# Optimization experiments

Hardware: AMD Instinct MI355X
Metric: run time of the kernel (lower is better)

The kernel has to match this reference:

```python
import jax, jax.numpy as jnp
import numpy as np

CM = 0.05   # collision_margin
NT = 4      # n_timesteps

def _lin(x, W, b):
    return x @ W + b

def _mlp2(x, W1, b1, W2, b2):
    return _lin(jax.nn.relu(_lin(x, W1, b1)), W2, b2)

def _mlp3(x, W1, b1, W2, b2, W3, b3):
    h = jax.nn.relu(_lin(x, W1, b1))
    h = jax.nn.relu(_lin(h, W2, b2))
    return _lin(h, W3, b3)

def _xavier(key, fan_in, fan_out):
    std = np.sqrt(2.0 / (fan_in + fan_out))
    return jax.random.normal(key, (fan_in, fan_out), dtype=jnp.float32) * std

def setup_inputs() -> dict:
    key = jax.random.key(0)
    ks = jax.random.split(key, 16)
    sd, h, es, ud, rd, gd = 8, 128, 128, 32, 64, 32
    B, N, T = 16, 64, 8
    inp = {
        'states': jax.random.normal(ks[0], (B, N, T, sd), dtype=jnp.float32),
        'temp': 1,
        # StateEncoder: Linear(sd,h)-ReLU-Linear(h,es)-ReLU
        'sW1': _xavier(ks[1], sd, h), 'sb1': jnp.zeros((h,), jnp.float32),
        'sW2': _xavier(ks[2], h, es), 'sb2': jnp.zeros((es,), jnp.float32),
        # InputEncoder (collision_margin path): Linear(sd,h)-ReLU-Linear(h,ud)
        'uW1': _xavier(ks[3], sd, h), 'ub1': jnp.zeros((h,), jnp.float32),
        'uW2': _xavier(ks[4], h, ud), 'ub2': jnp.zeros((ud,), jnp.float32),
        # InputPropagator: Linear(es+ud, ud)
        'upW': _xavier(ks[5], es + ud, ud), 'upb': jnp.zeros((ud,), jnp.float32),
        # RelationEncoder (collision_margin path): Linear(sd,h)-ReLU-Linear(h,rd)
        'reW1': _xavier(ks[6], sd, h), 'reb1': jnp.zeros((h,), jnp.float32),
        'reW2': _xavier(ks[7], h, rd), 'reb2': jnp.zeros((rd,), jnp.float32),
        # RelationPropagator: Linear(2*es+rd, rd)
        'rpW': _xavier(ks[8], 2 * es + rd, rd), 'rpb': jnp.zeros((rd,), jnp.float32),
        # ComposedEmbedding: Linear(es+ud+rd,h)-ReLU-Linear(h,h)-ReLU-Linear(h,gd)
        'cW1': _xavier(ks[9], es + ud + rd, h), 'cb1': jnp.zeros((h,), jnp.float32),
        'cW2': _xavier(ks[10], h, h), 'cb2': jnp.zeros((h,), jnp.float32),
        'cW3': _xavier(ks[11], h, gd), 'cb3': jnp.zeros((gd,), jnp.float32),
    }
    return inp

def reference(states, temp, sW1, sb1, sW2, sb2, uW1, ub1, uW2, ub2, upW, upb,
              reW1, reb1, reW2, reb2, rpW, rpb, cW1, cb1, cW2, cb2, cW3, cb3):
    B, N, T, sd = states.shape
    BT = B * T
    s = states.transpose(0, 2, 1, 3).reshape(BT, N, sd)  # [BT,N,sd]

    # node encoders
    enc_obj = jax.nn.relu(_mlp2(s, sW1, sb1, sW2, sb2))   # [BT,N,es]
    enc_u = _mlp2(s, uW1, ub1, uW2, ub2)                  # [BT,N,ud] (no relu in collision_margin path)
    # u mask (get_u_states_mask)
    u = ((jnp.abs(s[..., 0:1]) > 1 - CM) | (jnp.abs(s[..., NT:NT + 1]) > 1 - CM)).astype(s.dtype)

    obs_u = jax.nn.relu(_lin(jnp.concatenate([enc_obj, enc_u], axis=-1), upW, upb))  # [BT,N,ud]
    enc_comp = jnp.concatenate([enc_obj, obs_u], axis=-1)  # [BT,N,es+ud]

    # pairwise relations: receiver i (dim1), sender j (dim2)
    rel_states = s[:, :, None, :] - s[:, None, :, :]        # [BT,N,N,sd]
    enc_rel = jax.nn.relu(_mlp2(rel_states, reW1, reb1, reW2, reb2))  # [BT,N,N,rd]
    sel = ((jnp.abs(rel_states[..., 0:1]) > 2 * CM) |
           (jnp.abs(rel_states[..., NT:NT + 1]) > 2 * CM)).astype(s.dtype)  # [BT,N,N,1]

    es = enc_obj.shape[-1]
    recv = jnp.broadcast_to(enc_obj[:, :, None, :], (BT, N, N, es))
    send = jnp.broadcast_to(enc_obj[:, None, :, :], (BT, N, N, es))
    rel_in = jnp.concatenate([recv, send, enc_rel], axis=-1)            # [BT,N,N,2es+rd]
    rel_eff = jax.nn.relu(_lin(rel_in, rpW, rpb)) * sel                 # [BT,N,N,rd]
    rel_agg = rel_eff.sum(axis=2)                                       # scatter-sum over senders -> [BT,N,rd]

    enc_comp = jnp.concatenate([enc_comp, rel_agg], axis=-1)            # [BT,N,es+ud+rd]
    g = _mlp3(enc_comp, cW1, cb1, cW2, cb2, cW3, cb3)                   # [BT,N,gd]
    return g.reshape(B, T, N, -1)
```

## Files before the change

kernel.cpp:

```cpp
#include <hip/hip_runtime.h>
#include <hip/hip_bf16.h>


typedef __bf16 bf16x8 __attribute__((ext_vector_type(8)));
typedef _Float16 half8 __attribute__((ext_vector_type(8)));
typedef _Float16 half4 __attribute__((ext_vector_type(4)));
typedef float f32x4 __attribute__((ext_vector_type(4)));

static __device__ __forceinline__ half8 relu8(half8 x) {
    half8 z = {};
    return __builtin_elementwise_max(x, z);
}

__global__ __launch_bounds__(256) void k_prep(
    const float* __restrict__ sW1, const float* __restrict__ uW1,
    const float* __restrict__ reW1, const float* __restrict__ sW2,
    const float* __restrict__ uW2, const float* __restrict__ upW,
    const float* __restrict__ reW2, const float* __restrict__ rpW,
    const float* __restrict__ cW1, const float* __restrict__ cW2,
    const float* __restrict__ cW3,
    __bf16* __restrict__ Wl1f, __bf16* __restrict__ Ws2f,
    __bf16* __restrict__ Wu2f, __bf16* __restrict__ Wupf,
    __bf16* __restrict__ Wabf, _Float16* __restrict__ W2f,
    _Float16* __restrict__ Wbf, __bf16* __restrict__ Wc1f,
    __bf16* __restrict__ Wc2f, __bf16* __restrict__ Wc3f)
{
    const int tid  = blockIdx.x * 256 + threadIdx.x;
    const int nthr = gridDim.x * 256;

#define PACK(dst, CAST, NKT, NCT, EXPR)                             \
    for (int q = tid; q < (NKT) * (NCT) * 512; q += nthr) {         \
        const int f = q >> 9, rem = q & 511;                        \
        const int lane = rem >> 3, e = rem & 7;                     \
        const int kt = f / (NCT), ct = f % (NCT);                   \
        const int k = kt * 32 + (lane >> 4) * 8 + e;                \
        const int c = ct * 16 + (lane & 15);                        \
        (dst)[q] = (CAST)(EXPR);                                    \
        (void)k; (void)c;                                           \
    }

    PACK(Wl1f, __bf16, 1, 24, (k >= 8 ? 0.f :
        (c < 128 ? sW1[k * 128 + c] :
         c < 256 ? uW1[k * 128 + (c - 128)] : reW1[k * 128 + (c - 256)])))
    PACK(Ws2f, __bf16, 4, 8, sW2[k * 128 + c])
    PACK(Wu2f, __bf16, 4, 2, uW2[k * 32 + c])
    PACK(Wupf, __bf16, 5, 2, (k < 160 ? upW[k * 32 + c] : 0.f))
    PACK(Wabf, __bf16, 4, 8, (c < 64 ? rpW[k * 64 + c] : rpW[(128 + k) * 64 + (c - 64)]))
    PACK(W2f,  _Float16, 4, 4, reW2[k * 64 + c])
    PACK(Wbf,  _Float16, 2, 4, rpW[(256 + k) * 64 + c])
    PACK(Wc1f, __bf16, 7, 8, cW1[k * 128 + c])
    PACK(Wc2f, __bf16, 4, 8, cW2[k * 128 + c])
    PACK(Wc3f, __bf16, 4, 2, cW3[k * 32 + c])
#undef PACK
}

__global__ __launch_bounds__(512, 2) void k_mega(
    const float* __restrict__ states,
    const float* __restrict__ sb1, const float* __restrict__ sb2,
    const float* __restrict__ ub1, const float* __restrict__ ub2,
    const float* __restrict__ upb, const float* __restrict__ reb1,
    const float* __restrict__ reb2, const float* __restrict__ rpb,
    const float* __restrict__ cb1, const float* __restrict__ cb2,
    const float* __restrict__ cb3,
    const __bf16* __restrict__ Wl1f, const __bf16* __restrict__ Ws2f,
    const __bf16* __restrict__ Wu2f, const __bf16* __restrict__ Wupf,
    const __bf16* __restrict__ Wabf,
    const _Float16* __restrict__ W2f, const _Float16* __restrict__ Wbf,
    const __bf16* __restrict__ Wc1f, const __bf16* __restrict__ Wc2f,
    const __bf16* __restrict__ Wc3f,
    float* __restrict__ out)
{
    const int t    = threadIdx.x;
    const int lane = t & 63;
    const int w    = t >> 6;
    const int lr   = lane >> 4;
    const int lc   = lane & 15;
    const int bid  = (blockIdx.x & 7) * 64 + (blockIdx.x >> 3);
    const int bt   = bid >> 2;
    const int ig   = bid & 3;
    const int b    = bt >> 3, tstep = bt & 7;
    const int rowb = bt * 64 + ig * 16;

    __shared__ _Float16 s_pj[64 * 128];
    __shared__ _Float16 s_bmT[64 * 72];
    __shared__ float    s_ai[16 * 64];
    __shared__ __bf16   s_eo[64 * 128];
    __shared__ __bf16   s_scr[16 * 256];
    __shared__ __bf16   s_x[16 * 256];
    __shared__ __bf16   s_eu[16 * 40];
    __shared__ _Float16 s_rb[128];
    __shared__ float    s_s0[64], s_s4[64];

    if (t < 128) s_rb[t] = (_Float16)reb1[t];
    if (t < 64) {
        const float* sp = &states[((size_t)((b * 64 + t) * 8 + tstep)) * 8];
        s_s0[t] = sp[0];
        s_s4[t] = sp[4];
    }

    for (int rt = 0; rt < 4; ++rt) {
        bf16x8 af1 = {};
        if (lr == 0) {
            const int n = rt * 16 + lc;
            const float* sp = &states[((size_t)((b * 64 + n) * 8 + tstep)) * 8];
            const float4 v0 = *reinterpret_cast<const float4*>(sp);
            const float4 v1 = *reinterpret_cast<const float4*>(sp + 4);
            af1[0] = (__bf16)v0.x; af1[1] = (__bf16)v0.y;
            af1[2] = (__bf16)v0.z; af1[3] = (__bf16)v0.w;
            af1[4] = (__bf16)v1.x; af1[5] = (__bf16)v1.y;
            af1[6] = (__bf16)v1.z; af1[7] = (__bf16)v1.w;
        }
        const int nct = (rt == ig) ? 3 : 2;
        for (int ci = 0; ci < nct; ++ci) {
            const int ct = (ci < 2) ? (w * 2 + ci) : (16 + w);
            const int wl = (ct < 8) ? ct : (ct < 16 ? ct + 8 : ct - 8);
            const bf16x8 wf = *reinterpret_cast<const bf16x8*>(
                Wl1f + ((size_t)(wl * 64 + lane)) * 8);
            const float bias = (ct < 8) ? sb1[ct * 16 + lc]
                              : (ct >= 16) ? ub1[(ct - 16) * 16 + lc] : 0.f;
            f32x4 acc = {bias, bias, bias, bias};
            acc = __builtin_amdgcn_mfma_f32_16x16x32_bf16(af1, wf, acc, 0, 0, 0);
            #pragma unroll
            for (int r = 0; r < 4; ++r) {
                const int jj = lr * 4 + r;
                if (ct < 8) {
                    const int col = ct * 16 + lc, g = col >> 3;
                    s_scr[jj * 256 + (((g ^ (jj & 7)) << 3) | (col & 7))] =
                        (__bf16)fmaxf(acc[r], 0.f);
                } else if (ct < 16) {
                    const int col = (ct - 8) * 16 + lc, g = col >> 3;
                    const int j64 = rt * 16 + jj;
                    s_pj[j64 * 128 + ((g ^ (j64 & 7)) << 3) + (col & 7)] =
                        (_Float16)acc[r];
                } else {
                    const int col = 128 + (ct - 16) * 16 + lc, g = col >> 3;
                    s_scr[jj * 256 + (((g ^ (jj & 7)) << 3) | (col & 7))] =
                        (__bf16)fmaxf(acc[r], 0.f);
                }
            }
        }
        __syncthreads();

        {
            const int jr = lc, sw = lc & 7;
            bf16x8 h1f[4];
            #pragma unroll
            for (int kt = 0; kt < 4; ++kt)
                h1f[kt] = *reinterpret_cast<const bf16x8*>(
                    &s_scr[jr * 256 + (((kt * 4 + lr) ^ sw) << 3)]);
            const int ct = w;
            const float bias = sb2[ct * 16 + lc];
            f32x4 acc = {bias, bias, bias, bias};
            #pragma unroll
            for (int kt = 0; kt < 4; ++kt) {
                const bf16x8 wf = *reinterpret_cast<const bf16x8*>(
                    Ws2f + ((size_t)((kt * 8 + ct) * 64 + lane)) * 8);
                acc = __builtin_amdgcn_mfma_f32_16x16x32_bf16(h1f[kt], wf, acc, 0, 0, 0);
            }
            #pragma unroll
            for (int r = 0; r < 4; ++r) {
                const int jj = lr * 4 + r;
                const int j64 = rt * 16 + jj;
                const int col = ct * 16 + lc, g = col >> 3;
                const __bf16 v = (__bf16)fmaxf(acc[r], 0.f);
                s_eo[j64 * 128 + (((g ^ (j64 & 7)) << 3) | (col & 7))] = v;
                if (rt == ig)
                    s_x[jj * 256 + (((g ^ (jj & 7)) << 3) | (col & 7))] = v;
            }
            if (rt == ig && w < 2) {
                bf16x8 huf[4];
                #pragma unroll
                for (int kt = 0; kt < 4; ++kt)
                    huf[kt] = *reinterpret_cast<const bf16x8*>(
                        &s_scr[jr * 256 + (((16 + kt * 4 + lr) ^ sw) << 3)]);
                const float bias2 = ub2[w * 16 + lc];
                f32x4 acc2 = {bias2, bias2, bias2, bias2};
                #pragma unroll
                for (int kt = 0; kt < 4; ++kt) {
                    const bf16x8 wf = *reinterpret_cast<const bf16x8*>(
                        Wu2f + ((size_t)((kt * 2 + w) * 64 + lane)) * 8);
                    acc2 = __builtin_amdgcn_mfma_f32_16x16x32_bf16(huf[kt], wf, acc2, 0, 0, 0);
                }
                #pragma unroll
                for (int r = 0; r < 4; ++r)
                    s_eu[(lr * 4 + r) * 40 + w * 16 + lc] = (__bf16)acc2[r];
            }
        }
        __syncthreads();
    }

    {
        #pragma unroll
        for (int q = 0; q < 2; ++q) {
            const int task = w * 2 + q;
            const int rt2 = task >> 2;
            const int ct = 4 + (task & 3);
            const int j64 = rt2 * 16 + lc, so = j64 & 7;
            bf16x8 eof[4];
            #pragma unroll
            for (int kt = 0; kt < 4; ++kt)
                eof[kt] = *reinterpret_cast<const bf16x8*>(
                    &s_eo[j64 * 128 + (((kt * 4 + lr) ^ so) << 3)]);
            f32x4 acc = {0.f, 0.f, 0.f, 0.f};
            #pragma unroll
            for (int kt = 0; kt < 4; ++kt) {
                const bf16x8 wf = *reinterpret_cast<const bf16x8*>(
                    Wabf + ((size_t)((kt * 8 + ct) * 64 + lane)) * 8);
                acc = __builtin_amdgcn_mfma_f32_16x16x32_bf16(eof[kt], wf, acc, 0, 0, 0);
            }
            #pragma unroll
            for (int r = 0; r < 4; ++r)
                s_bmT[((ct - 4) * 16 + lc) * 72 + rt2 * 16 + lr * 4 + r] =
                    (_Float16)acc[r];
        }
        const int jo = ig * 16 + lc, so2 = jo & 7;
        if (w < 4) {
            bf16x8 eof[4];
            #pragma unroll
            for (int kt = 0; kt < 4; ++kt)
                eof[kt] = *reinterpret_cast<const bf16x8*>(
                    &s_eo[jo * 128 + (((kt * 4 + lr) ^ so2) << 3)]);
            f32x4 acc = {0.f, 0.f, 0.f, 0.f};
            #pragma unroll
            for (int kt = 0; kt < 4; ++kt) {
                const bf16x8 wf = *reinterpret_cast<const bf16x8*>(
                    Wabf + ((size_t)((kt * 8 + w) * 64 + lane)) * 8);
                acc = __builtin_amdgcn_mfma_f32_16x16x32_bf16(eof[kt], wf, acc, 0, 0, 0);
            }
            #pragma unroll
            for (int r = 0; r < 4; ++r) {
                const int col = w * 16 + lc;
                s_ai[(lr * 4 + r) * 64 + col] = acc[r] + rpb[col];
            }
        } else if (w < 6) {
            const int ct = w - 4;
            bf16x8 eof[5];
            #pragma unroll
            for (int kt = 0; kt < 4; ++kt)
                eof[kt] = *reinterpret_cast<const bf16x8*>(
                    &s_eo[jo * 128 + (((kt * 4 + lr) ^ so2) << 3)]);
            eof[4] = *reinterpret_cast<const bf16x8*>(&s_eu[lc * 40 + lr * 8]);
            const float bias = upb[ct * 16 + lc];
            f32x4 acc = {bias, bias, bias, bias};
            #pragma unroll
            for (int kt = 0; kt < 5; ++kt) {
                const bf16x8 wf = *reinterpret_cast<const bf16x8*>(
                    Wupf + ((size_t)((kt * 2 + ct) * 64 + lane)) * 8);
                acc = __builtin_amdgcn_mfma_f32_16x16x32_bf16(eof[kt], wf, acc, 0, 0, 0);
            }
            #pragma unroll
            for (int r = 0; r < 4; ++r) {
                const int jj = lr * 4 + r;
                const int col = 128 + ct * 16 + lc, g = col >> 3;
                s_x[jj * 256 + (((g ^ (jj & 7)) << 3) | (col & 7))] =
                    (__bf16)fmaxf(acc[r], 0.f);
            }
        }
    }
    __syncthreads();

    half8 w2f[4][4];
    #pragma unroll
    for (int kt = 0; kt < 4; ++kt)
        #pragma unroll
        for (int ct = 0; ct < 4; ++ct)
            w2f[kt][ct] = *reinterpret_cast<const half8*>(
                W2f + ((size_t)((kt * 4 + ct) * 64 + lane)) * 8);
    half8 wbf[2][4];
    #pragma unroll
    for (int kt = 0; kt < 2; ++kt)
        #pragma unroll
        for (int ct = 0; ct < 4; ++ct)
            wbf[kt][ct] = *reinterpret_cast<const half8*>(
                Wbf + ((size_t)((kt * 4 + ct) * 64 + lane)) * 8);
    float reb2c[4];
    #pragma unroll
    for (int ct = 0; ct < 4; ++ct) reb2c[ct] = reb2[ct * 16 + lc];

    _Float16* er = reinterpret_cast<_Float16*>(s_eo) + w * (16 * 64);
    float rag2[2][4];

    for (int q = 0; q < 2; ++q) {
        const int il = w * 2 + q;
        const int i  = ig * 16 + il;
        const int isw = i & 7;

        half8 pib[4];
        #pragma unroll
        for (int kt = 0; kt < 4; ++kt) {
            const int g = kt * 4 + lr;
            const half8 pv = *reinterpret_cast<const half8*>(
                &s_pj[i * 128 + ((g ^ isw) << 3)]);
            const half8 rb = *reinterpret_cast<const half8*>(&s_rb[g * 8]);
            pib[kt] = pv + rb;
        }
        float aic[4];
        #pragma unroll
        for (int ct = 0; ct < 4; ++ct) aic[ct] = s_ai[il * 64 + ct * 16 + lc];
        const unsigned long long selm = __ballot(
            fabsf(s_s0[i] - s_s0[lane]) > 0.1f ||
            fabsf(s_s4[i] - s_s4[lane]) > 0.1f);

        float ragg[4] = {0.f, 0.f, 0.f, 0.f};

        for (int jt = 0; jt < 4; ++jt) {
            const int j = jt * 16 + lc;
            const int jsw = j & 7;
            half8 af[4];
            #pragma unroll
            for (int kt = 0; kt < 4; ++kt) {
                const int g = (kt * 4 + lr) ^ jsw;
                const half8 pj = *reinterpret_cast<const half8*>(
                    &s_pj[j * 128 + (g << 3)]);
                af[kt] = relu8(pib[kt] - pj);
            }
            #pragma unroll
            for (int ct = 0; ct < 4; ++ct) {
                f32x4 acc = {reb2c[ct], reb2c[ct], reb2c[ct], reb2c[ct]};
                #pragma unroll
                for (int kt = 0; kt < 4; ++kt)
                    acc = __builtin_amdgcn_mfma_f32_16x16x32_f16(
                        af[kt], w2f[kt][ct], acc, 0, 0, 0);
                #pragma unroll
                for (int r = 0; r < 4; ++r) {
                    const int jj2 = lr * 4 + r;
                    const int c = ct * 16 + lc;
                    er[jj2 * 64 + ((((c >> 3) ^ (jj2 & 7)) << 3) | (c & 7))] =
                        (_Float16)fmaxf(acc[r], 0.f);
                }
            }
            half8 a2[2];
            #pragma unroll
            for (int kt = 0; kt < 2; ++kt) {
                const int g = (kt * 4 + lr) ^ (lc & 7);
                a2[kt] = *reinterpret_cast<const half8*>(&er[lc * 64 + (g << 3)]);
            }
            #pragma unroll
            for (int ct = 0; ct < 4; ++ct) {
                const half4 bm4 = *reinterpret_cast<const half4*>(
                    &s_bmT[(ct * 16 + lc) * 72 + jt * 16 + lr * 4]);
                f32x4 acc = {aic[ct] + (float)bm4[0], aic[ct] + (float)bm4[1],
                             aic[ct] + (float)bm4[2], aic[ct] + (float)bm4[3]};
                #pragma unroll
                for (int kt = 0; kt < 2; ++kt)
                    acc = __builtin_amdgcn_mfma_f32_16x16x32_f16(
                        a2[kt], wbf[kt][ct], acc, 0, 0, 0);
                #pragma unroll
                for (int r = 0; r < 4; ++r) {
                    const int jj = jt * 16 + lr * 4 + r;
                    float v = fmaxf(acc[r], 0.f);
                    v = ((selm >> jj) & 1ull) ? v : 0.f;
                    ragg[ct] += v;
                }
            }
        }
        #pragma unroll
        for (int ct = 0; ct < 4; ++ct) {
            ragg[ct] += __shfl_xor(ragg[ct], 16);
            ragg[ct] += __shfl_xor(ragg[ct], 32);
            rag2[q][ct] = ragg[ct];
        }
    }
    if (lr == 0) {
        #pragma unroll
        for (int q = 0; q < 2; ++q) {
            const int il = w * 2 + q;
            #pragma unroll
            for (int ct = 0; ct < 4; ++ct) {
                const int c = ct * 16 + lc;
                const int gg = 20 + (c >> 3);
                s_x[il * 256 + ((gg ^ (il & 7)) << 3) + (c & 7)] =
                    (__bf16)rag2[q][ct];
            }
        }
    }
    __syncthreads();

    __bf16* s_h1 = s_scr;
    __bf16* s_h2 = s_scr + 16 * 128;

    const int jr = lc;
    const int sw = lc & 7;
    bf16x8 xf[7];
    #pragma unroll
    for (int kt = 0; kt < 7; ++kt)
        xf[kt] = *reinterpret_cast<const bf16x8*>(
            &s_x[jr * 256 + (((kt * 4 + lr) ^ sw) << 3)]);
    {
        const int ct = w;
        const float bias = cb1[ct * 16 + lc];
        f32x4 acc = {bias, bias, bias, bias};
        #pragma unroll
        for (int kt = 0; kt < 7; ++kt) {
            const bf16x8 wf = *reinterpret_cast<const bf16x8*>(
                Wc1f + ((size_t)((kt * 8 + ct) * 64 + lane)) * 8);
            acc = __builtin_amdgcn_mfma_f32_16x16x32_bf16(xf[kt], wf, acc, 0, 0, 0);
        }
        #pragma unroll
        for (int r = 0; r < 4; ++r) {
            const int jj = lr * 4 + r;
            const int col = ct * 16 + lc, g = col >> 3;
            s_h1[jj * 128 + (((g ^ (jj & 7)) << 3) | (col & 7))] =
                (__bf16)fmaxf(acc[r], 0.f);
        }
    }
    __syncthreads();

    {
        bf16x8 hf[4];
        #pragma unroll
        for (int kt = 0; kt < 4; ++kt)
            hf[kt] = *reinterpret_cast<const bf16x8*>(
                &s_h1[jr * 128 + (((kt * 4 + lr) ^ sw) << 3)]);
        const int ct = w;
        const float bias = cb2[ct * 16 + lc];
        f32x4 acc = {bias, bias, bias, bias};
        #pragma unroll
        for (int kt = 0; kt < 4; ++kt) {
            const bf16x8 wf = *reinterpret_cast<const bf16x8*>(
                Wc2f + ((size_t)((kt * 8 + ct) * 64 + lane)) * 8);
            acc = __builtin_amdgcn_mfma_f32_16x16x32_bf16(hf[kt], wf, acc, 0, 0, 0);
        }
        #pragma unroll
        for (int r = 0; r < 4; ++r) {
            const int jj = lr * 4 + r;
            const int col = ct * 16 + lc, g = col >> 3;
            s_h2[jj * 128 + (((g ^ (jj & 7)) << 3) | (col & 7))] =
                (__bf16)fmaxf(acc[r], 0.f);
        }
    }
    __syncthreads();

    if (w < 2) {
        bf16x8 h2f[4];
        #pragma unroll
        for (int kt = 0; kt < 4; ++kt)
            h2f[kt] = *reinterpret_cast<const bf16x8*>(
                &s_h2[jr * 128 + (((kt * 4 + lr) ^ sw) << 3)]);
        const int ct = w;
        const float bias = cb3[ct * 16 + lc];
        f32x4 acc = {bias, bias, bias, bias};
        #pragma unroll
        for (int kt = 0; kt < 4; ++kt) {
            const bf16x8 wf = *reinterpret_cast<const bf16x8*>(
                Wc3f + ((size_t)((kt * 2 + ct) * 64 + lane)) * 8);
            acc = __builtin_amdgcn_mfma_f32_16x16x32_bf16(h2f[kt], wf, acc, 0, 0, 0);
        }
        #pragma unroll
        for (int r = 0; r < 4; ++r) {
            const int rg = rowb + lr * 4 + r;
            out[(size_t)rg * 32 + ct * 16 + lc] = acc[r];
        }
    }
}

extern "C" void kernel_launch(void* const* d_in, const int* in_sizes, int n_in,
                              void* d_out, int out_size, void* d_ws, size_t ws_size,
                              hipStream_t stream) {
    const float* states = (const float*)d_in[0];
    const float* sW1  = (const float*)d_in[2];
    const float* sb1  = (const float*)d_in[3];
    const float* sW2  = (const float*)d_in[4];
    const float* sb2  = (const float*)d_in[5];
    const float* uW1  = (const float*)d_in[6];
    const float* ub1  = (const float*)d_in[7];
    const float* uW2  = (const float*)d_in[8];
    const float* ub2  = (const float*)d_in[9];
    const float* upW  = (const float*)d_in[10];
    const float* upb  = (const float*)d_in[11];
    const float* reW1 = (const float*)d_in[12];
    const float* reb1 = (const float*)d_in[13];
    const float* reW2 = (const float*)d_in[14];
    const float* reb2 = (const float*)d_in[15];
    const float* rpW  = (const float*)d_in[16];
    const float* rpb  = (const float*)d_in[17];
    const float* cW1  = (const float*)d_in[18];
    const float* cb1  = (const float*)d_in[19];
    const float* cW2  = (const float*)d_in[20];
    const float* cb2  = (const float*)d_in[21];
    const float* cW3  = (const float*)d_in[22];
    const float* cb3  = (const float*)d_in[23];
    float* out = (float*)d_out;

    _Float16* W2f  = (_Float16*)d_ws;
    _Float16* Wbf  = W2f + 16 * 512;
    __bf16* Wl1f = (__bf16*)(Wbf + 8 * 512);
    __bf16* Ws2f = Wl1f + 24 * 512;
    __bf16* Wu2f = Ws2f + 32 * 512;
    __bf16* Wupf = Wu2f + 8 * 512;
    __bf16* Wabf = Wupf + 10 * 512;
    __bf16* Wc1f = Wabf + 32 * 512;
    __bf16* Wc2f = Wc1f + 56 * 512;
    __bf16* Wc3f = Wc2f + 32 * 512;

    k_prep<<<64, 256, 0, stream>>>(sW1, uW1, reW1, sW2, uW2, upW, reW2, rpW,
                                   cW1, cW2, cW3,
                                   Wl1f, Ws2f, Wu2f, Wupf, Wabf, W2f, Wbf,
                                   Wc1f, Wc2f, Wc3f);
    k_mega<<<512, 512, 0, stream>>>(states, sb1, sb2, ub1, ub2, upb,
                                    reb1, reb2, rpb, cb1, cb2, cb3,
                                    Wl1f, Ws2f, Wu2f, Wupf, Wabf, W2f, Wbf,
                                    Wc1f, Wc2f, Wc3f, out);
}
```

Baseline: 152.2 us.

## Double-buffer node-encoder scratch, pad LDS rows, stage Wb weights in LDS

Replaces the separate shared arrays with one manually laid-out LDS block and double-buffers the encoder scratch. The next row tile's first layer now runs alongside the current tile's second layer, halving the barriers in the node-encoder loop. Swizzled LDS indexing for s_pj and the per-wave relation scratch is replaced by padded row strides. The rpW tail fragments are read from LDS instead of being held in registers, which cuts register pressure. s_setprio is also raised around the pairwise MFMA loop, at the cost of more LDS traffic and possible bank conflicts from the padded layout.

Result: faster. 146.2 us (-3.9%).

```diff
diff --git a/kernel.cpp b/kernel.cpp
--- a/kernel.cpp
+++ b/kernel.cpp
@@ -53,6 +53,19 @@
     PACK(Wc3f, __bf16, 4, 2, cW3[k * 32 + c])
 #undef PACK
 }
+
+constexpr int OFF_PJ   = 0;
+constexpr int OFF_BMT  = 17408;
+constexpr int OFF_AI   = 26624;
+constexpr int OFF_EO   = 30720;
+constexpr int OFF_SCRA = 47104;
+constexpr int OFF_SCRB = 55296;
+constexpr int OFF_X    = 63488;
+constexpr int OFF_EU   = 71680;
+constexpr int OFF_RB   = 72960;
+constexpr int OFF_S0   = 73216;
+constexpr int OFF_S4   = 73472;
+constexpr int LDS_SZ   = 73728;
 
 __global__ __launch_bounds__(512, 2) void k_mega(
     const float* __restrict__ states,
@@ -70,6 +83,8 @@
     const __bf16* __restrict__ Wc3f,
     float* __restrict__ out)
 {
+    __shared__ __align__(16) char lds[LDS_SZ];
+
     const int t    = threadIdx.x;
     const int lane = t & 63;
     const int w    = t >> 6;
@@ -81,24 +96,26 @@
     const int b    = bt >> 3, tstep = bt & 7;
     const int rowb = bt * 64 + ig * 16;
 
-    __shared__ _Float16 s_pj[64 * 128];
-    __shared__ _Float16 s_bmT[64 * 72];
-    __shared__ float    s_ai[16 * 64];
-    __shared__ __bf16   s_eo[64 * 128];
-    __shared__ __bf16   s_scr[16 * 256];
-    __shared__ __bf16   s_x[16 * 256];
-    __shared__ __bf16   s_eu[16 * 40];
-    __shared__ _Float16 s_rb[128];
-    __shared__ float    s_s0[64], s_s4[64];
-
-    if (t < 128) s_rb[t] = (_Float16)reb1[t];
+    _Float16* s_pjh = (_Float16*)(lds + OFF_PJ);
+    _Float16* s_bmT = (_Float16*)(lds + OFF_BMT);
+    float*    s_ai  = (float*)(lds + OFF_AI);
+    __bf16*   s_eo  = (__bf16*)(lds + OFF_EO);
+    __bf16*   scrA  = (__bf16*)(lds + OFF_SCRA);
+    __bf16*   scrB  = (__bf16*)(lds + OFF_SCRB);
+    __bf16*   s_x   = (__bf16*)(lds + OFF_X);
+    __bf16*   s_eu  = (__bf16*)(lds + OFF_EU);
+    _Float16* s_rbh = (_Float16*)(lds + OFF_RB);
+    float*    s_s0  = (float*)(lds + OFF_S0);
+    float*    s_s4  = (float*)(lds + OFF_S4);
+
+    if (t < 128) s_rbh[t] = (_Float16)reb1[t];
     if (t < 64) {
         const float* sp = &states[((size_t)((b * 64 + t) * 8 + tstep)) * 8];
         s_s0[t] = sp[0];
         s_s4[t] = sp[4];
     }
 
-    for (int rt = 0; rt < 4; ++rt) {
+    auto do_N1 = [&](int rt, __bf16* scr) {
         bf16x8 af1 = {};
         if (lr == 0) {
             const int n = rt * 16 + lc;
@@ -125,67 +142,72 @@
                 const int jj = lr * 4 + r;
                 if (ct < 8) {
                     const int col = ct * 16 + lc, g = col >> 3;
-                    s_scr[jj * 256 + (((g ^ (jj & 7)) << 3) | (col & 7))] =
+                    scr[jj * 256 + (((g ^ (jj & 7)) << 3) | (col & 7))] =
                         (__bf16)fmaxf(acc[r], 0.f);
                 } else if (ct < 16) {
-                    const int col = (ct - 8) * 16 + lc, g = col >> 3;
-                    const int j64 = rt * 16 + jj;
-                    s_pj[j64 * 128 + ((g ^ (j64 & 7)) << 3) + (col & 7)] =
+                    s_pjh[(rt * 16 + jj) * 136 + (ct - 8) * 16 + lc] =
                         (_Float16)acc[r];
                 } else {
                     const int col = 128 + (ct - 16) * 16 + lc, g = col >> 3;
-                    s_scr[jj * 256 + (((g ^ (jj & 7)) << 3) | (col & 7))] =
+                    scr[jj * 256 + (((g ^ (jj & 7)) << 3) | (col & 7))] =
                         (__bf16)fmaxf(acc[r], 0.f);
                 }
             }
         }
-        __syncthreads();
-
-        {
-            const int jr = lc, sw = lc & 7;
-            bf16x8 h1f[4];
+    };
+    auto do_N2 = [&](int rt, __bf16* scr) {
+        const int jr = lc, sw = lc & 7;
+        bf16x8 h1f[4];
+        #pragma unroll
+        for (int kt = 0; kt < 4; ++kt)
+            h1f[kt] = *reinterpret_cast<const bf16x8*>(
+                &scr[jr * 256 + (((kt * 4 + lr) ^ sw) << 3)]);
+        const int ct = w;
+        const float bias = sb2[ct * 16 + lc];
+        f32x4 acc = {bias, bias, bias, bias};
+        #pragma unroll
+        for (int kt = 0; kt < 4; ++kt) {
+            const bf16x8 wf = *reinterpret_cast<const bf16x8*>(
+                Ws2f + ((size_t)((kt * 8 + ct) * 64 + lane)) * 8);
+            acc = __builtin_amdgcn_mfma_f32_16x16x32_bf16(h1f[kt], wf, acc, 0, 0, 0);
+        }
+        #pragma unroll
+        for (int r = 0; r < 4; ++r) {
+            const int jj = lr * 4 + r;
+            const int j64 = rt * 16 + jj;
+            const int col = ct * 16 + lc, g = col >> 3;
+            const __bf16 v = (__bf16)fmaxf(acc[r], 0.f);
+            s_eo[j64 * 128 + (((g ^ (j64 & 7)) << 3) | (col & 7))] = v;
+            if (rt == ig)
+                s_x[jj * 256 + (((g ^ (jj & 7)) << 3) | (col & 7))] = v;
+        }
+        if (rt == ig && w < 2) {
+            bf16x8 huf[4];
             #pragma unroll
             for (int kt = 0; kt < 4; ++kt)
-                h1f[kt] = *reinterpret_cast<const bf16x8*>(
-                    &s_scr[jr * 256 + (((kt * 4 + lr) ^ sw) << 3)]);
-            const int ct = w;
-            const float bias = sb2[ct * 16 + lc];
-            f32x4 acc = {bias, bias, bias, bias};
+                huf[kt] = *reinterpret_cast<const bf16x8*>(
+                    &scr[jr * 256 + (((16 + kt * 4 + lr) ^ sw) << 3)]);
+            const float bias2 = ub2[w * 16 + lc];
+            f32x4 acc2 = {bias2, bias2, bias2, bias2};
             #pragma unroll
             for (int kt = 0; kt < 4; ++kt) {
                 const bf16x8 wf = *reinterpret_cast<const bf16x8*>(
-                    Ws2f + ((size_t)((kt * 8 + ct) * 64 + lane)) * 8);
-                acc = __builtin_amdgcn_mfma_f32_16x16x32_bf16(h1f[kt], wf, acc, 0, 0, 0);
-            }
-            #pragma unroll
-            for (int r = 0; r < 4; ++r) {
-                const int jj = lr * 4 + r;
-                const int j64 = rt * 16 + jj;
-                const int col = ct * 16 + lc, g = col >> 3;
-                const __bf16 v = (__bf16)fmaxf(acc[r], 0.f);
-                s_eo[j64 * 128 + (((g ^ (j64 & 7)) << 3) | (col & 7))] = v;
-                if (rt == ig)
-                    s_x[jj * 256 + (((g ^ (jj & 7)) << 3) | (col & 7))] = v;
-            }
-            if (rt == ig && w < 2) {
-                bf16x8 huf[4];
-                #pragma unroll
-                for (int kt = 0; kt < 4; ++kt)
-                    huf[kt] = *reinterpret_cast<const bf16x8*>(
-                        &s_scr[jr * 256 + (((16 + kt * 4 + lr) ^ sw) << 3)]);
-                const float bias2 = ub2[w * 16 + lc];
-                f32x4 acc2 = {bias2, bias2, bias2, bias2};
-                #pragma unroll
-                for (int kt = 0; kt < 4; ++kt) {
-                    const bf16x8 wf = *reinterpret_cast<const bf16x8*>(
-                        Wu2f + ((size_t)((kt * 2 + w) * 64 + lane)) * 8);
-                    acc2 = __builtin_amdgcn_mfma_f32_16x16x32_bf16(huf[kt], wf, acc2, 0, 0, 0);
-                }
-                #pragma unroll
-                for (int r = 0; r < 4; ++r)
-                    s_eu[(lr * 4 + r) * 40 + w * 16 + lc] = (__bf16)acc2[r];
-            }
-        }
+                    Wu2f + ((size_t)((kt * 2 + w) * 64 + lane)) * 8);
+                acc2 = __builtin_amdgcn_mfma_f32_16x16x32_bf16(huf[kt], wf, acc2, 0, 0, 0);
+            }
+            #pragma unroll
+            for (int r = 0; r < 4; ++r)
+                s_eu[(lr * 4 + r) * 40 + w * 16 + lc] = (__bf16)acc2[r];
+        }
+    };
+
+    do_N1(0, scrA);
+    __syncthreads();
+    for (int rt = 0; rt < 4; ++rt) {
+        __bf16* cur = (rt & 1) ? scrB : scrA;
+        __bf16* nxt = (rt & 1) ? scrA : scrB;
+        do_N2(rt, cur);
+        if (rt < 3) do_N1(rt + 1, nxt);
         __syncthreads();
     }
 
@@ -256,6 +278,8 @@
                     (__bf16)fmaxf(acc[r], 0.f);
             }
         }
+        *reinterpret_cast<half8*>((_Float16*)scrB + t * 8) =
+            *reinterpret_cast<const half8*>(Wbf + t * 8);
     }
     __syncthreads();
 
@@ -266,34 +290,26 @@
         for (int ct = 0; ct < 4; ++ct)
             w2f[kt][ct] = *reinterpret_cast<const half8*>(
                 W2f + ((size_t)((kt * 4 + ct) * 64 + lane)) * 8);
-    half8 wbf[2][4];
-    #pragma unroll
-    for (int kt = 0; kt < 2; ++kt)
-        #pragma unroll
-        for (int ct = 0; ct < 4; ++ct)
-            wbf[kt][ct] = *reinterpret_cast<const half8*>(
-                Wbf + ((size_t)((kt * 4 + ct) * 64 + lane)) * 8);
     float reb2c[4];
     #pragma unroll
     for (int ct = 0; ct < 4; ++ct) reb2c[ct] = reb2[ct * 16 + lc];
 
-    _Float16* er = reinterpret_cast<_Float16*>(s_eo) + w * (16 * 64);
+    const _Float16* wbl = (const _Float16*)scrB;
+    _Float16* er = (_Float16*)s_eo + w * (16 * 88);
+    const int erw = (lr * 4) * 88 + lc;
+    const int erd = lc * 88 + lr * 8;
     float rag2[2][4];
 
     for (int q = 0; q < 2; ++q) {
         const int il = w * 2 + q;
         const int i  = ig * 16 + il;
-        const int isw = i & 7;
-
+
+        const _Float16* pirow = s_pjh + i * 136;
         half8 pib[4];
         #pragma unroll
-        for (int kt = 0; kt < 4; ++kt) {
-            const int g = kt * 4 + lr;
-            const half8 pv = *reinterpret_cast<const half8*>(
-                &s_pj[i * 128 + ((g ^ isw) << 3)]);
-            const half8 rb = *reinterpret_cast<const half8*>(&s_rb[g * 8]);
-            pib[kt] = pv + rb;
-        }
+        for (int kt = 0; kt < 4; ++kt)
+            pib[kt] = *reinterpret_cast<const half8*>(pirow + kt * 32 + lr * 8)
+                    + *reinterpret_cast<const half8*>(s_rbh + kt * 32 + lr * 8);
         float aic[4];
         #pragma unroll
         for (int ct = 0; ct < 4; ++ct) aic[ct] = s_ai[il * 64 + ct * 16 + lc];
@@ -304,16 +320,13 @@
         float ragg[4] = {0.f, 0.f, 0.f, 0.f};
 
         for (int jt = 0; jt < 4; ++jt) {
-            const int j = jt * 16 + lc;
-            const int jsw = j & 7;
+            const _Float16* pjr = s_pjh + (jt * 16 + lc) * 136 + lr * 8;
+            __builtin_amdgcn_s_setprio(1);
             half8 af[4];
             #pragma unroll
-            for (int kt = 0; kt < 4; ++kt) {
-                const int g = (kt * 4 + lr) ^ jsw;
-                const half8 pj = *reinterpret_cast<const half8*>(
-                    &s_pj[j * 128 + (g << 3)]);
-                af[kt] = relu8(pib[kt] - pj);
-            }
+            for (int kt = 0; kt < 4; ++kt)
+                af[kt] = relu8(pib[kt] -
+                    *reinterpret_cast<const half8*>(pjr + kt * 32));
             #pragma unroll
             for (int ct = 0; ct < 4; ++ct) {
                 f32x4 acc = {reb2c[ct], reb2c[ct], reb2c[ct], reb2c[ct]};
@@ -322,29 +335,26 @@
                     acc = __builtin_amdgcn_mfma_f32_16x16x32_f16(
                         af[kt], w2f[kt][ct], acc, 0, 0, 0);
                 #pragma unroll
-                for (int r = 0; r < 4; ++r) {
-                    const int jj2 = lr * 4 + r;
-                    const int c = ct * 16 + lc;
-                    er[jj2 * 64 + ((((c >> 3) ^ (jj2 & 7)) << 3) | (c & 7))] =
-                        (_Float16)fmaxf(acc[r], 0.f);
-                }
+                for (int r = 0; r < 4; ++r)
+                    er[erw + r * 88 + ct * 16] = (_Float16)fmaxf(acc[r], 0.f);
             }
             half8 a2[2];
             #pragma unroll
-            for (int kt = 0; kt < 2; ++kt) {
-                const int g = (kt * 4 + lr) ^ (lc & 7);
-                a2[kt] = *reinterpret_cast<const half8*>(&er[lc * 64 + (g << 3)]);
-            }
+            for (int kt = 0; kt < 2; ++kt)
+                a2[kt] = *reinterpret_cast<const half8*>(er + erd + kt * 32);
             #pragma unroll
             for (int ct = 0; ct < 4; ++ct) {
                 const half4 bm4 = *reinterpret_cast<const half4*>(
-                    &s_bmT[(ct * 16 + lc) * 72 + jt * 16 + lr * 4]);
+                    s_bmT + (ct * 16 + lc) * 72 + jt * 16 + lr * 4);
                 f32x4 acc = {aic[ct] + (float)bm4[0], aic[ct] + (float)bm4[1],
                              aic[ct] + (float)bm4[2], aic[ct] + (float)bm4[3]};
                 #pragma unroll
-                for (int kt = 0; kt < 2; ++kt)
+                for (int kt = 0; kt < 2; ++kt) {
+                    const half8 wf = *reinterpret_cast<const half8*>(
+                        wbl + ((kt * 4 + ct) * 64 + lane) * 8);
                     acc = __builtin_amdgcn_mfma_f32_16x16x32_f16(
-                        a2[kt], wbf[kt][ct], acc, 0, 0, 0);
+                        a2[kt], wf, acc, 0, 0, 0);
+                }
                 #pragma unroll
                 for (int r = 0; r < 4; ++r) {
                     const int jj = jt * 16 + lr * 4 + r;
@@ -353,6 +363,7 @@
                     ragg[ct] += v;
                 }
             }
+            __builtin_amdgcn_s_setprio(0);
         }
         #pragma unroll
         for (int ct = 0; ct < 4; ++ct) {
@@ -376,8 +387,8 @@
     }
     __syncthreads();
 
-    __bf16* s_h1 = s_scr;
-    __bf16* s_h2 = s_scr + 16 * 128;
+    __bf16* s_h1 = scrA;
+    __bf16* s_h2 = scrB;
 
     const int jr = lc;
     const int sw = lc & 7;
```
